# Kernel tuning notes

Hardware: AMD Instinct MI355X
Metric: run time of the kernel (lower is better)

The kernel has to match this reference:

```python
import jax, jax.numpy as jnp
import numpy as np

B, N, F_IN, F_OUT = 32, 1024, 256, 256
K_NEIGHBORS = 64
TEMPERATURE = 1.0
LN_EPS = 1e-5


def setup_inputs() -> dict:
    key = jax.random.key(0)
    ks = jax.random.split(key, 10)
    s_in = 1.0 / np.sqrt(F_IN)
    s_out = 1.0 / np.sqrt(F_OUT)
    # learned static adjacency: 0.1 everywhere + 0.9 on diagonal (self loops)
    static_edge_weights = jnp.full((N, N), 0.1, dtype=jnp.float32) + 0.9 * jnp.eye(N, dtype=jnp.float32)
    return {
        "x": jax.random.normal(ks[0], (B, N, F_IN), dtype=jnp.float32),
        "wq": jax.random.uniform(ks[1], (F_IN, F_OUT), jnp.float32, -s_in, s_in),
        "bq": jnp.zeros((F_OUT,), jnp.float32),
        "wk": jax.random.uniform(ks[2], (F_IN, F_OUT), jnp.float32, -s_in, s_in),
        "bk": jnp.zeros((F_OUT,), jnp.float32),
        "wv": jax.random.uniform(ks[3], (F_IN, F_OUT), jnp.float32, -s_in, s_in),
        "bv": jnp.zeros((F_OUT,), jnp.float32),
        "static_edge_weights": static_edge_weights,
        "w1": jax.random.uniform(ks[4], (F_OUT, F_OUT), jnp.float32, -s_out, s_out),
        "b1": jnp.zeros((F_OUT,), jnp.float32),
        "ln_g": jnp.ones((F_OUT,), jnp.float32),
        "ln_b": jnp.zeros((F_OUT,), jnp.float32),
        "w2": jax.random.uniform(ks[5], (F_OUT, F_OUT), jnp.float32, -s_out, s_out),
        "b2": jnp.zeros((F_OUT,), jnp.float32),
    }


def reference(x, wq, bq, wk, bk, wv, bv, static_edge_weights, w1, b1, ln_g, ln_b, w2, b2):
    Bc, Nc, _ = x.shape
    q = jnp.einsum("bnf,fo->bno", x, wq) + bq
    k = jnp.einsum("bnf,fo->bno", x, wk) + bk
    v = jnp.einsum("bnf,fo->bno", x, wv) + bv
    # [B, N, N] attention scores with learned static adjacency bias
    scores = jnp.einsum("bnd,bmd->bnm", q, k) / jnp.sqrt(jnp.float32(F_OUT))
    scores = scores + static_edge_weights[None, :, :]
    # top-k sparsification along last dim
    _, topk_idx = jax.lax.top_k(scores, K_NEIGHBORS)  # [B, N, K]
    bi = jnp.arange(Bc)[:, None, None]
    ni = jnp.arange(Nc)[None, :, None]
    mask = jnp.zeros(scores.shape, dtype=bool).at[bi, ni, topk_idx].set(True)
    scores = jnp.where(mask, scores, jnp.float32(-1e9))
    attn = jax.nn.softmax(scores / TEMPERATURE, axis=-1)
    messages = jnp.einsum("bnm,bmd->bnd", attn, v)
    # out_mlp: Linear -> LayerNorm -> ReLU -> Linear
    h = jnp.einsum("bnd,de->bne", messages, w1) + b1
    mu = jnp.mean(h, axis=-1, keepdims=True)
    var = jnp.mean(jnp.square(h - mu), axis=-1, keepdims=True)
    h = (h - mu) / jnp.sqrt(var + LN_EPS) * ln_g + ln_b
    h = jax.nn.relu(h)
    h = jnp.einsum("bnd,de->bne", h, w2) + b2
    out = h + v  # residual
    return (out, attn)
```

## Files before the change

### kernel.cpp

```cpp
#include <hip/hip_runtime.h>
#include <cstdint>

#define NB 32
#define NNODES 1024
#define DD 256
#define KNB 64
#define MTOT (NB * NNODES)

#define INV65536 1.52587890625e-05f
#define KCELL 2.44140625e-4f

typedef _Float16 half8 __attribute__((ext_vector_type(8)));
typedef _Float16 half4 __attribute__((ext_vector_type(4)));
typedef float f32x4 __attribute__((ext_vector_type(4)));

typedef __attribute__((address_space(3))) uint32_t lds_u32;
typedef __attribute__((address_space(1))) uint32_t glb_u32;

__device__ __forceinline__ void gll16(const _Float16* g, _Float16* l) {
  __builtin_amdgcn_global_load_lds((const glb_u32*)g, (lds_u32*)l, 16, 0, 0);
}

__device__ __forceinline__ void split2(float v, _Float16& h, _Float16& l) {
  h = (_Float16)v;
  l = (_Float16)(v - (float)h);
}

__global__ __launch_bounds__(256) void prep_w(const float* __restrict__ wq,
                                              const float* __restrict__ wk,
                                              const float* __restrict__ wv,
                                              const float* __restrict__ w1,
                                              const float* __restrict__ w2,
                                              _Float16* __restrict__ WT) {
  const int idx = blockIdx.x * 256 + threadIdx.x;
  const int wsel = idx >> 16;
  const int rem = idx & 65535;
  const int k = rem >> 8, n = rem & 255;
  const float* src = (wsel == 0) ? wq : (wsel == 1) ? wk : (wsel == 2) ? wv : (wsel == 3) ? w1 : w2;
  const float v = src[rem] * 1024.0f;
  _Float16 h1, h2;
  split2(v, h1, h2);
  WT[(size_t)wsel * 131072 + n * 256 + k] = h1;
  WT[(size_t)wsel * 131072 + 65536 + n * 256 + k] = h2;
}

__global__ __launch_bounds__(256) void prep_x(const float* __restrict__ x,
                                              _Float16* __restrict__ X1,
                                              _Float16* __restrict__ X2) {
  const size_t i = ((size_t)blockIdx.x * 256 + threadIdx.x) * 8;
  const float4 a = *(const float4*)(x + i);
  const float4 bb = *(const float4*)(x + i + 4);
  const float vals[8] = {a.x, a.y, a.z, a.w, bb.x, bb.y, bb.z, bb.w};
  half8 h, l;
#pragma unroll
  for (int e = 0; e < 8; ++e) {
    _Float16 hh, ll;
    split2(vals[e] * 64.0f, hh, ll);
    h[e] = hh;
    l[e] = ll;
  }
  *(half8*)(X1 + i) = h;
  *(half8*)(X2 + i) = l;
}

#define SWZ_OFF(r, cc) ((r) * 64 + (((cc) ^ ((r)&7)) << 3))

__global__ __launch_bounds__(256) void gemm_qkv(const _Float16* __restrict__ X1,
                                                const _Float16* __restrict__ X2,
                                                const _Float16* __restrict__ WT,
                                                const float* __restrict__ bq,
                                                const float* __restrict__ bk,
                                                const float* __restrict__ bv,
                                                _Float16* __restrict__ Q1, _Float16* __restrict__ Q2,
                                                _Float16* __restrict__ K1, _Float16* __restrict__ K2,
                                                _Float16* __restrict__ V16) {
  __shared__ _Float16 sm[4 * 8192];
  _Float16* sA1 = sm;
  _Float16* sA2 = sm + 8192;
  _Float16* sB1 = sm + 16384;
  _Float16* sB2 = sm + 24576;

  const int tid = threadIdx.x;
  const int lane = tid & 63, w = tid >> 6;
  const int r16 = lane & 15, kg = lane >> 4;
  const int rsub = lane >> 3, csub = lane & 7;
  const int wm = (w >> 1) * 64, wn = (w & 1) * 64;

  const int id = blockIdx.x;
  const int c8 = id & 7, t = id >> 3;
  const int gy = (t / 6) * 8 + c8;
  const int j6 = t % 6;
  const int wsel = j6 >> 1;
  const int n0 = (j6 & 1) * 128;
  const int m0 = gy * 128;
  const bool full = (wsel != 2);

  const _Float16* pB1 = WT + (size_t)wsel * 131072;
  const _Float16* pB2 = pB1 + 65536;

  f32x4 acc[4][4];
#pragma unroll
  for (int i = 0; i < 4; ++i)
#pragma unroll
    for (int j = 0; j < 4; ++j) acc[i][j] = f32x4{0.f, 0.f, 0.f, 0.f};

  for (int k0 = 0; k0 < DD; k0 += 64) {
    __syncthreads();
#pragma unroll
    for (int it = 0; it < 4; ++it) {
      const int r = (w << 5) + (it << 3) + rsub;
      const int swz = ((csub ^ (r & 7)) << 3);
      const int ldso = (w << 11) + (it << 9);
      gll16(X1 + (size_t)(m0 + r) * DD + k0 + swz, sA1 + ldso);
      gll16(pB1 + (size_t)(n0 + r) * DD + k0 + swz, sB1 + ldso);
      if (full) {
        gll16(X2 + (size_t)(m0 + r) * DD + k0 + swz, sA2 + ldso);
        gll16(pB2 + (size_t)(n0 + r) * DD + k0 + swz, sB2 + ldso);
      }
    }
    __syncthreads();

#pragma unroll
    for (int s = 0; s < 2; ++s) {
      half8 aA[4], aB[4], bA[4], bB[4];
#pragma unroll
      for (int mi = 0; mi < 4; ++mi) {
        const int off = SWZ_OFF(wm + mi * 16 + r16, s * 4 + kg);
        aA[mi] = *(const half8*)(sA1 + off);
      }
#pragma unroll
      for (int nj = 0; nj < 4; ++nj) {
        const int off = SWZ_OFF(wn + nj * 16 + r16, s * 4 + kg);
        bA[nj] = *(const half8*)(sB1 + off);
      }
      if (full) {
#pragma unroll
        for (int mi = 0; mi < 4; ++mi) {
          const int off = SWZ_OFF(wm + mi * 16 + r16, s * 4 + kg);
          aB[mi] = *(const half8*)(sA2 + off);
        }
#pragma unroll
        for (int nj = 0; nj < 4; ++nj) {
          const int off = SWZ_OFF(wn + nj * 16 + r16, s * 4 + kg);
          bB[nj] = *(const half8*)(sB2 + off);
        }
      }
#pragma unroll
      for (int mi = 0; mi < 4; ++mi)
#pragma unroll
        for (int nj = 0; nj < 4; ++nj) {
          acc[mi][nj] = __builtin_amdgcn_mfma_f32_16x16x32_f16(aA[mi], bA[nj], acc[mi][nj], 0, 0, 0);
          if (full) {
            acc[mi][nj] = __builtin_amdgcn_mfma_f32_16x16x32_f16(aA[mi], bB[nj], acc[mi][nj], 0, 0, 0);
            acc[mi][nj] = __builtin_amdgcn_mfma_f32_16x16x32_f16(aB[mi], bA[nj], acc[mi][nj], 0, 0, 0);
          }
        }
    }
  }

  const float* bsel = (wsel == 0) ? bq : (wsel == 1) ? bk : bv;
  _Float16* P1 = (wsel == 0) ? Q1 : K1;
  _Float16* P2 = (wsel == 0) ? Q2 : K2;
#pragma unroll
  for (int mi = 0; mi < 4; ++mi)
#pragma unroll
    for (int nj = 0; nj < 4; ++nj) {
      const int col = n0 + wn + nj * 16 + r16;
#pragma unroll
      for (int j = 0; j < 4; ++j) {
        const int rr = m0 + wm + mi * 16 + kg * 4 + j;
        if (wsel == 2) {
          V16[(size_t)rr * DD + col] = (_Float16)(acc[mi][nj][j] * INV65536 + bsel[col]);
        } else {
          const float qv = acc[mi][nj][j] * (1.0f / 1024.0f) + 64.0f * bsel[col];
          _Float16 h1, h2;
          split2(qv, h1, h2);
          P1[(size_t)rr * DD + col] = h1;
          P2[(size_t)rr * DD + col] = h2;
        }
      }
    }
}

template <int EPI>
__global__ __launch_bounds__(256) void gemm_split(const _Float16* __restrict__ A1,
                                                  const _Float16* __restrict__ B1g,
                                                  const _Float16* __restrict__ B2g,
                                                  const float* __restrict__ bias,
                                                  const _Float16* __restrict__ resid16,
                                                  float* __restrict__ C,
                                                  _Float16* __restrict__ C16) {
  __shared__ _Float16 sm[3 * 8192];
  _Float16* sA1 = sm;
  _Float16* sB1 = sm + 8192;
  _Float16* sB2 = sm + 16384;

  const int tid = threadIdx.x;
  const int lane = tid & 63, w = tid >> 6;
  const int r16 = lane & 15, kg = lane >> 4;
  const int rsub = lane >> 3, csub = lane & 7;
  const int wm = (w >> 1) * 64, wn = (w & 1) * 64;

  const int n0 = blockIdx.x * 128;
  const int m0 = blockIdx.y * 128;

  const _Float16* pB1 = B1g;
  const _Float16* pB2 = B2g;
  if (EPI == 2) {
    const size_t boff = (size_t)(m0 >> 10) * NNODES * DD;
    pB1 += boff;
    pB2 += boff;
  }

  f32x4 acc[4][4];
#pragma unroll
  for (int i = 0; i < 4; ++i)
#pragma unroll
    for (int j = 0; j < 4; ++j) acc[i][j] = f32x4{0.f, 0.f, 0.f, 0.f};

  for (int k0 = 0; k0 < DD; k0 += 64) {
    __syncthreads();
#pragma unroll
    for (int it = 0; it < 4; ++it) {
      const int r = (w << 5) + (it << 3) + rsub;
      const int swz = ((csub ^ (r & 7)) << 3);
      const int ldso = (w << 11) + (it << 9);
      gll16(A1 + (size_t)(m0 + r) * DD + k0 + swz, sA1 + ldso);
      gll16(pB1 + (size_t)(n0 + r) * DD + k0 + swz, sB1 + ldso);
      gll16(pB2 + (size_t)(n0 + r) * DD + k0 + swz, sB2 + ldso);
    }
    __syncthreads();

#pragma unroll
    for (int s = 0; s < 2; ++s) {
      half8 aA[4], bA[4], bB[4];
#pragma unroll
      for (int mi = 0; mi < 4; ++mi) {
        const int off = SWZ_OFF(wm + mi * 16 + r16, s * 4 + kg);
        aA[mi] = *(const half8*)(sA1 + off);
      }
#pragma unroll
      for (int nj = 0; nj < 4; ++nj) {
        const int off = SWZ_OFF(wn + nj * 16 + r16, s * 4 + kg);
        bA[nj] = *(const half8*)(sB1 + off);
        bB[nj] = *(const half8*)(sB2 + off);
      }
#pragma unroll
      for (int mi = 0; mi < 4; ++mi)
#pragma unroll
        for (int nj = 0; nj < 4; ++nj) {
          acc[mi][nj] = __builtin_amdgcn_mfma_f32_16x16x32_f16(aA[mi], bA[nj], acc[mi][nj], 0, 0, 0);
          acc[mi][nj] = __builtin_amdgcn_mfma_f32_16x16x32_f16(aA[mi], bB[nj], acc[mi][nj], 0, 0, 0);
        }
    }
  }

#pragma unroll
  for (int mi = 0; mi < 4; ++mi)
#pragma unroll
    for (int nj = 0; nj < 4; ++nj) {
      const int col = n0 + wn + nj * 16 + r16;
#pragma unroll
      for (int j = 0; j < 4; ++j) {
        const int rr = m0 + wm + mi * 16 + kg * 4 + j;
        const float v = acc[mi][nj][j] * INV65536;
        if (EPI == 2) {
          const float sv = v + bias[(size_t)(rr & (NNODES - 1)) * NNODES + col];
          const float f = fminf(fmaxf((sv + 8.0f) * 4096.0f, 0.0f), 65535.0f);
          uint16_t* kbase = (uint16_t*)((char*)C + (size_t)rr * 4096 + 2048);
          kbase[col] = (uint16_t)(unsigned)f;
        } else if (EPI == 0) {
          C16[(size_t)rr * DD + col] = (_Float16)(v + bias[col]);
        } else {
          C[(size_t)rr * DD + col] = v + bias[col] + (float)resid16[(size_t)rr * DD + col];
        }
      }
    }
}

__global__ __launch_bounds__(256, 4) void topk_softmax_msg(float* __restrict__ S,
                                                           const _Float16* __restrict__ V16,
                                                           const _Float16* __restrict__ Q1,
                                                           const _Float16* __restrict__ Q2,
                                                           const _Float16* __restrict__ K1,
                                                           const _Float16* __restrict__ K2,
                                                           const float* __restrict__ adj,
                                                           _Float16* __restrict__ M1) {
  const int tid = threadIdx.x;
  const int w = tid >> 6, lane = tid & 63;
  const int id = blockIdx.x;
  const int xcd = id & 7, t = id >> 3;
  const int b = (t >> 8) * 8 + xcd;
  const int row = b * NNODES + (t & 255) * 4 + w;
  const int m = row & (NNODES - 1);
  float* Srow = S + (size_t)row * NNODES;
  const uint16_t* krow = (const uint16_t*)((const char*)S + (size_t)row * 4096 + 2048);

  __shared__ float2 spair[4][KNB];
  __shared__ int cidxs[4][32];
  __shared__ float cex[4][32];
  __shared__ int csel[4][32];

  if (lane < KNB) spair[w][lane] = make_float2(0.0f, __int_as_float(0));

  const uint4 u0 = *(const uint4*)(krow + lane * 8);
  const uint4 u1 = *(const uint4*)(krow + 512 + lane * 8);
  int k[16];
  {
    const unsigned uu[8] = {u0.x, u0.y, u0.z, u0.w, u1.x, u1.y, u1.z, u1.w};
#pragma unroll
    for (int q = 0; q < 8; ++q) {
      k[q * 2] = (int)(uu[q] & 0xffffu);
      k[q * 2 + 1] = (int)(uu[q] >> 16);
    }
  }

  float st[16];
#pragma unroll
  for (int t2 = 0; t2 < 16; ++t2) st[t2] = fmaf((float)k[t2] + 0.5f, KCELL, -8.0f);

  int cur = 0;
#pragma unroll 1
  for (int bit = 15; bit >= 0; --bit) {
    const int cand = cur | (1 << bit);
    int cnt = 0;
#pragma unroll
    for (int t2 = 0; t2 < 16; ++t2) cnt += (int)__popcll(__ballot(k[t2] >= cand));
    if (cnt >= KNB) cur = cand;
  }

  const int kHi = cur + 5;
  const int kLo = cur - 4;

  const unsigned long long ltmask = (1ull << lane) - 1ull;
  unsigned hm = 0u, cm = 0u;
  int cpos[16];
  int nhi = 0, ncand = 0;
#pragma unroll
  for (int g = 0; g < 2; ++g) {
    bool hiv[8], cdv[8];
    unsigned long long mh[8], mc[8];
#pragma unroll
    for (int e = 0; e < 8; ++e) {
      const int t2 = g * 8 + e;
      hiv[e] = (k[t2] >= kHi);
      cdv[e] = (!hiv[e]) && (k[t2] >= kLo);
      mh[e] = __ballot(hiv[e]);
      mc[e] = __ballot(cdv[e]);
    }
    int below = 0, tot_h = 0, tot_c = 0;
#pragma unroll
    for (int e = 0; e < 8; ++e) {
      below += (int)__popcll(mc[e] & ltmask);
      tot_h += (int)__popcll(mh[e]);
      tot_c += (int)__popcll(mc[e]);
    }
    int own = 0;
#pragma unroll
    for (int e = 0; e < 8; ++e) {
      const int t2 = g * 8 + e;
      cpos[t2] = -1;
      if (hiv[e]) hm |= (1u << t2);
      if (cdv[e]) {
        cm |= (1u << t2);
        const int p = ncand + below + own;
        cpos[t2] = p;
        if (p < 32) cidxs[w][p] = g * 512 + lane * 8 + e;
        ++own;
      }
    }
    nhi += tot_h;
    ncand += tot_c;
  }
  const int need = KNB - nhi;

  unsigned selm;
  if (ncand == need) {
    selm = hm | cm;
  } else {
    const int nc = (ncand <= 32) ? ncand : 32;
    const int nd = (need <= nc) ? need : nc;
    const size_t qoff = (size_t)row * DD + lane * 4;
    const half4 q1v = *(const half4*)(Q1 + qoff);
    const half4 q2v = *(const half4*)(Q2 + qoff);
    float qf[4];
#pragma unroll
    for (int e = 0; e < 4; ++e) qf[e] = (float)q1v[e] + (float)q2v[e];
    const float* adjrow = adj + (size_t)m * NNODES;
#pragma unroll 2
    for (int t2 = 0; t2 < nc; ++t2) {
      const int j = cidxs[w][t2];
      const size_t koff = ((size_t)b * NNODES + j) * DD + lane * 4;
      const half4 k1v = *(const half4*)(K1 + koff);
      const half4 k2v = *(const half4*)(K2 + koff);
      float part = 0.0f;
#pragma unroll
      for (int e = 0; e < 4; ++e) part = fmaf(qf[e], (float)k1v[e] + (float)k2v[e], part);
#pragma unroll
      for (int off = 32; off > 0; off >>= 1) part += __shfl_xor(part, off);
      if (lane == 0) cex[w][t2] = part * INV65536 + adjrow[j];
    }
    if (lane < nc) {
      const float et = cex[w][lane];
      int rank = 0;
      for (int u = 0; u < nc; ++u) {
        const float eu = cex[w][u];
        rank += (eu > et || (eu == et && u < lane)) ? 1 : 0;
      }
      csel[w][lane] = (rank < nd) ? 1 : 0;
    }
    selm = hm;
#pragma unroll
    for (int t2 = 0; t2 < 16; ++t2) {
      if (((cm >> t2) & 1u) && cpos[t2] >= 0 && cpos[t2] < 32 && csel[w][cpos[t2]]) selm |= (1u << t2);
    }
  }

  float rmax = st[0];
#pragma unroll
  for (int t2 = 1; t2 < 16; ++t2) rmax = fmaxf(rmax, st[t2]);
#pragma unroll
  for (int off = 32; off > 0; off >>= 1) rmax = fmaxf(rmax, __shfl_xor(rmax, off));

  float p[16];
  float sum = 0.0f;
#pragma unroll
  for (int t2 = 0; t2 < 16; ++t2) {
    p[t2] = __expf(st[t2] - rmax);
    if ((selm >> t2) & 1u) sum += p[t2];
  }
#pragma unroll
  for (int off = 32; off > 0; off >>= 1) sum += __shfl_xor(sum, off);
  const float inv = 1.0f / sum;

  int run = 0;
#pragma unroll
  for (int g = 0; g < 2; ++g) {
    bool sel8[8];
    unsigned long long ms[8];
#pragma unroll
    for (int e = 0; e < 8; ++e) {
      sel8[e] = (selm >> (g * 8 + e)) & 1u;
      ms[e] = __ballot(sel8[e]);
    }
    int below = 0, tot = 0;
#pragma unroll
    for (int e = 0; e < 8; ++e) {
      below += (int)__popcll(ms[e] & ltmask);
      tot += (int)__popcll(ms[e]);
    }
    float ow[8];
    int own = 0;
#pragma unroll
    for (int e = 0; e < 8; ++e) {
      const int t2 = g * 8 + e;
      const float aw = sel8[e] ? p[t2] * inv : 0.0f;
      ow[e] = aw;
      if (sel8[e]) {
        const int pos = run + below + own;
        if (pos < KNB)
          spair[w][pos] = make_float2(aw, __int_as_float((g * 512 + lane * 8 + e) * (DD * 2)));
        ++own;
      }
    }
    float* dst = Srow + g * 512 + lane * 8;
    *(float4*)(dst) = make_float4(ow[0], ow[1], ow[2], ow[3]);
    *(float4*)(dst + 4) = make_float4(ow[4], ow[5], ow[6], ow[7]);
    run += tot;
  }

  float4 acc = {0.0f, 0.0f, 0.0f, 0.0f};
  const char* Vbase = (const char*)(V16 + (size_t)b * NNODES * DD) + lane * 8;
#pragma unroll 4
  for (int t2 = 0; t2 < KNB; ++t2) {
    const float2 pr = spair[w][t2];
    const int off = __float_as_int(pr.y);
    const half4 vv = *(const half4*)(Vbase + off);
    acc.x = fmaf(pr.x, (float)vv[0], acc.x);
    acc.y = fmaf(pr.x, (float)vv[1], acc.y);
    acc.z = fmaf(pr.x, (float)vv[2], acc.z);
    acc.w = fmaf(pr.x, (float)vv[3], acc.w);
  }
  half4 m1;
  m1[0] = (_Float16)(acc.x * 64.0f);
  m1[1] = (_Float16)(acc.y * 64.0f);
  m1[2] = (_Float16)(acc.z * 64.0f);
  m1[3] = (_Float16)(acc.w * 64.0f);
  *(half4*)(M1 + (size_t)row * DD + lane * 4) = m1;
}

__global__ __launch_bounds__(256) void ln_relu(const _Float16* __restrict__ H16,
                                               const float* __restrict__ g,
                                               const float* __restrict__ bta,
                                               _Float16* __restrict__ H1) {
  const int tid = threadIdx.x;
  const int row = blockIdx.x * 4 + (tid >> 6);
  const int lane = tid & 63;
  const half4 hv = *(const half4*)(H16 + (size_t)row * DD + lane * 4);
  float h[4];
#pragma unroll
  for (int j = 0; j < 4; ++j) h[j] = (float)hv[j];

  float s = h[0] + h[1] + h[2] + h[3];
#pragma unroll
  for (int off = 32; off > 0; off >>= 1) s += __shfl_xor(s, off);
  const float mu = s * (1.0f / 256.0f);

  float d[4], sq = 0.0f;
#pragma unroll
  for (int j = 0; j < 4; ++j) {
    d[j] = h[j] - mu;
    sq += d[j] * d[j];
  }
#pragma unroll
  for (int off = 32; off > 0; off >>= 1) sq += __shfl_xor(sq, off);
  const float rstd = 1.0f / sqrtf(sq * (1.0f / 256.0f) + 1e-5f);

  const float4 gv = *(const float4*)(g + lane * 4);
  const float4 bv = *(const float4*)(bta + lane * 4);
  const float gg[4] = {gv.x, gv.y, gv.z, gv.w};
  const float bb[4] = {bv.x, bv.y, bv.z, bv.w};
  half4 o;
#pragma unroll
  for (int j = 0; j < 4; ++j) {
    const float y = fmaxf(d[j] * rstd * gg[j] + bb[j], 0.0f);
    o[j] = (_Float16)(y * 64.0f);
  }
  *(half4*)(H1 + (size_t)row * DD + lane * 4) = o;
}

extern "C" void kernel_launch(void* const* d_in, const int* in_sizes, int n_in,
                              void* d_out, int out_size, void* d_ws, size_t ws_size,
                              hipStream_t stream) {
  (void)in_sizes; (void)n_in; (void)out_size; (void)ws_size;
  const float* x   = (const float*)d_in[0];
  const float* wq  = (const float*)d_in[1];
  const float* bq  = (const float*)d_in[2];
  const float* wk  = (const float*)d_in[3];
  const float* bk  = (const float*)d_in[4];
  const float* wv  = (const float*)d_in[5];
  const float* bv  = (const float*)d_in[6];
  const float* adj = (const float*)d_in[7];
  const float* w1  = (const float*)d_in[8];
  const float* b1  = (const float*)d_in[9];
  const float* lng = (const float*)d_in[10];
  const float* lnb = (const float*)d_in[11];
  const float* w2  = (const float*)d_in[12];
  const float* b2  = (const float*)d_in[13];

  const size_t BND = (size_t)MTOT * DD;
  float* outp  = (float*)d_out;
  float* attnp = outp + BND;

  _Float16* X1 = (_Float16*)attnp;
  _Float16* X2 = X1 + BND;

  _Float16* Q1 = (_Float16*)d_ws;
  _Float16* Q2 = Q1 + BND;
  _Float16* K1 = Q2 + BND;
  _Float16* K2 = K1 + BND;
  _Float16* WT = K2 + BND;
  _Float16* V16 = WT + 5 * 131072;

  _Float16* M1 = Q1;
  _Float16* H16 = (_Float16*)K1;
  _Float16* H1 = Q1;

  const dim3 blk(256);

  prep_w<<<dim3(1280), blk, 0, stream>>>(wq, wk, wv, w1, w2, WT);
  prep_x<<<dim3(4096), blk, 0, stream>>>(x, X1, X2);
  gemm_qkv<<<dim3(1536), blk, 0, stream>>>(X1, X2, WT, bq, bk, bv, Q1, Q2, K1, K2, V16);
  gemm_split<2><<<dim3(8, 256), blk, 0, stream>>>(Q1, K1, K2, adj, nullptr, attnp, nullptr);
  topk_softmax_msg<<<dim3(MTOT / 4), blk, 0, stream>>>(attnp, V16, Q1, Q2, K1, K2, adj, M1);
  gemm_split<0><<<dim3(2, 256), blk, 0, stream>>>(M1, WT + 3 * 131072, WT + 3 * 131072 + 65536,
                                                  b1, nullptr, nullptr, H16);
  ln_relu<<<dim3(MTOT / 4), blk, 0, stream>>>(H16, lng, lnb, H1);
  gemm_split<1><<<dim3(2, 256), blk, 0, stream>>>(H1, WT + 4 * 131072, WT + 4 * 131072 + 65536,
                                                  b2, V16, outp, nullptr);
}
```

Baseline: 304.7 us.

## Remap score GEMM blocks per XCD and slim top-k selection register use

The score GEMM now uses a 1D grid whose block IDs are remapped so that each batch's tiles land on the same XCD, which should improve L2 reuse of K and adj. In the top-k kernel, the float score array is dropped: the softmax max is taken as an integer max over quantized keys, and exponentials are computed from key differences. Candidate position compaction now runs only in the rare tie-break path. The launch-bounds hint is replaced with waves_per_eu(4,4), aiming to cut register pressure and the ballot work done on the common path.

Result: slower. 324.0 us (+6.3%).

```diff
diff --git a/kernel.cpp b/kernel.cpp
--- a/kernel.cpp
+++ b/kernel.cpp
@@ -201,8 +201,19 @@
   const int rsub = lane >> 3, csub = lane & 7;
   const int wm = (w >> 1) * 64, wn = (w & 1) * 64;
 
-  const int n0 = blockIdx.x * 128;
-  const int m0 = blockIdx.y * 128;
+  int n0, m0;
+  if (EPI == 2) {
+    const int id = blockIdx.x;
+    const int c8 = id & 7, t = id >> 3;
+    const int Bb = ((t >> 6) << 3) + c8;
+    const int r = (t >> 3) & 7;
+    const int bx = t & 7;
+    n0 = bx * 128;
+    m0 = (Bb * 8 + r) * 128;
+  } else {
+    n0 = blockIdx.x * 128;
+    m0 = blockIdx.y * 128;
+  }
 
   const _Float16* pB1 = B1g;
   const _Float16* pB2 = B2g;
@@ -278,14 +289,15 @@
     }
 }
 
-__global__ __launch_bounds__(256, 4) void topk_softmax_msg(float* __restrict__ S,
-                                                           const _Float16* __restrict__ V16,
-                                                           const _Float16* __restrict__ Q1,
-                                                           const _Float16* __restrict__ Q2,
-                                                           const _Float16* __restrict__ K1,
-                                                           const _Float16* __restrict__ K2,
-                                                           const float* __restrict__ adj,
-                                                           _Float16* __restrict__ M1) {
+__global__ __launch_bounds__(256) __attribute__((amdgpu_waves_per_eu(4, 4)))
+void topk_softmax_msg(float* __restrict__ S,
+                      const _Float16* __restrict__ V16,
+                      const _Float16* __restrict__ Q1,
+                      const _Float16* __restrict__ Q2,
+                      const _Float16* __restrict__ K1,
+                      const _Float16* __restrict__ K2,
+                      const float* __restrict__ adj,
+                      _Float16* __restrict__ M1) {
   const int tid = threadIdx.x;
   const int w = tid >> 6, lane = tid & 63;
   const int id = blockIdx.x;
@@ -315,10 +327,6 @@
     }
   }
 
-  float st[16];
-#pragma unroll
-  for (int t2 = 0; t2 < 16; ++t2) st[t2] = fmaf((float)k[t2] + 0.5f, KCELL, -8.0f);
-
   int cur = 0;
 #pragma unroll 1
   for (int bit = 15; bit >= 0; --bit) {
@@ -332,45 +340,25 @@
   const int kHi = cur + 5;
   const int kLo = cur - 4;
 
-  const unsigned long long ltmask = (1ull << lane) - 1ull;
+  int kx = k[0];
+#pragma unroll
+  for (int t2 = 1; t2 < 16; ++t2) kx = (k[t2] > kx) ? k[t2] : kx;
+#pragma unroll
+  for (int off = 32; off > 0; off >>= 1) {
+    const int o = __shfl_xor(kx, off);
+    kx = (o > kx) ? o : kx;
+  }
+
   unsigned hm = 0u, cm = 0u;
-  int cpos[16];
   int nhi = 0, ncand = 0;
 #pragma unroll
-  for (int g = 0; g < 2; ++g) {
-    bool hiv[8], cdv[8];
-    unsigned long long mh[8], mc[8];
-#pragma unroll
-    for (int e = 0; e < 8; ++e) {
-      const int t2 = g * 8 + e;
-      hiv[e] = (k[t2] >= kHi);
-      cdv[e] = (!hiv[e]) && (k[t2] >= kLo);
-      mh[e] = __ballot(hiv[e]);
-      mc[e] = __ballot(cdv[e]);
-    }
-    int below = 0, tot_h = 0, tot_c = 0;
-#pragma unroll
-    for (int e = 0; e < 8; ++e) {
-      below += (int)__popcll(mc[e] & ltmask);
-      tot_h += (int)__popcll(mh[e]);
-      tot_c += (int)__popcll(mc[e]);
-    }
-    int own = 0;
-#pragma unroll
-    for (int e = 0; e < 8; ++e) {
-      const int t2 = g * 8 + e;
-      cpos[t2] = -1;
-      if (hiv[e]) hm |= (1u << t2);
-      if (cdv[e]) {
-        cm |= (1u << t2);
-        const int p = ncand + below + own;
-        cpos[t2] = p;
-        if (p < 32) cidxs[w][p] = g * 512 + lane * 8 + e;
-        ++own;
-      }
-    }
-    nhi += tot_h;
-    ncand += tot_c;
+  for (int t2 = 0; t2 < 16; ++t2) {
+    const bool hiv = (k[t2] >= kHi);
+    const bool cdv = (!hiv) && (k[t2] >= kLo);
+    if (hiv) hm |= (1u << t2);
+    if (cdv) cm |= (1u << t2);
+    nhi += (int)__popcll(__ballot(hiv));
+    ncand += (int)__popcll(__ballot(cdv));
   }
   const int need = KNB - nhi;
 
@@ -378,6 +366,38 @@
   if (ncand == need) {
     selm = hm | cm;
   } else {
+    const unsigned long long ltm = (1ull << lane) - 1ull;
+    int cpos[16];
+    int nc0 = 0;
+#pragma unroll
+    for (int g = 0; g < 2; ++g) {
+      bool cdv8[8];
+      unsigned long long mcv[8];
+#pragma unroll
+      for (int e = 0; e < 8; ++e) {
+        cdv8[e] = (cm >> (g * 8 + e)) & 1u;
+        mcv[e] = __ballot(cdv8[e]);
+      }
+      int below = 0, tot = 0;
+#pragma unroll
+      for (int e = 0; e < 8; ++e) {
+        below += (int)__popcll(mcv[e] & ltm);
+        tot += (int)__popcll(mcv[e]);
+      }
+      int own = 0;
+#pragma unroll
+      for (int e = 0; e < 8; ++e) {
+        const int t2 = g * 8 + e;
+        cpos[t2] = -1;
+        if (cdv8[e]) {
+          const int p2 = nc0 + below + own;
+          cpos[t2] = p2;
+          if (p2 < 32) cidxs[w][p2] = g * 512 + lane * 8 + e;
+          ++own;
+        }
+      }
+      nc0 += tot;
+    }
     const int nc = (ncand <= 32) ? ncand : 32;
     const int nd = (need <= nc) ? need : nc;
     const size_t qoff = (size_t)row * DD + lane * 4;
@@ -416,23 +436,18 @@
     }
   }
 
-  float rmax = st[0];
-#pragma unroll
-  for (int t2 = 1; t2 < 16; ++t2) rmax = fmaxf(rmax, st[t2]);
-#pragma unroll
-  for (int off = 32; off > 0; off >>= 1) rmax = fmaxf(rmax, __shfl_xor(rmax, off));
-
   float p[16];
   float sum = 0.0f;
 #pragma unroll
   for (int t2 = 0; t2 < 16; ++t2) {
-    p[t2] = __expf(st[t2] - rmax);
+    p[t2] = __expf((float)(k[t2] - kx) * KCELL);
     if ((selm >> t2) & 1u) sum += p[t2];
   }
 #pragma unroll
   for (int off = 32; off > 0; off >>= 1) sum += __shfl_xor(sum, off);
   const float inv = 1.0f / sum;
 
+  const unsigned long long ltmask = (1ull << lane) - 1ull;
   int run = 0;
 #pragma unroll
   for (int g = 0; g < 2; ++g) {
@@ -571,7 +586,7 @@
   prep_w<<<dim3(1280), blk, 0, stream>>>(wq, wk, wv, w1, w2, WT);
   prep_x<<<dim3(4096), blk, 0, stream>>>(x, X1, X2);
   gemm_qkv<<<dim3(1536), blk, 0, stream>>>(X1, X2, WT, bq, bk, bv, Q1, Q2, K1, K2, V16);
-  gemm_split<2><<<dim3(8, 256), blk, 0, stream>>>(Q1, K1, K2, adj, nullptr, attnp, nullptr);
+  gemm_split<2><<<dim3(2048), blk, 0, stream>>>(Q1, K1, K2, adj, nullptr, attnp, nullptr);
   topk_softmax_msg<<<dim3(MTOT / 4), blk, 0, stream>>>(attnp, V16, Q1, Q2, K1, K2, adj, M1);
   gemm_split<0><<<dim3(2, 256), blk, 0, stream>>>(M1, WT + 3 * 131072, WT + 3 * 131072 + 65536,
                                                   b1, nullptr, nullptr, H16);
```
